# Optimization experiments

Measured on AMD Instinct MI355X. Metric: run time of the kernel, lower is better.

The kernel has to match this reference:

```python
import jax, jax.numpy as jnp
import numpy as np

B, H, W = 4, 512, 512
CIN, COUT = 3, 3
K = CIN + COUT  # 6x6 per-pixel Gaussian covariance factors


def setup_inputs() -> dict:
    key = jax.random.key(0)
    ks = jax.random.split(key, 6)
    x = jax.random.normal(ks[0], (B, CIN, H, W), jnp.float32)
    y = jax.random.normal(ks[1], (B, COUT, H, W), jnp.float32)
    m = jax.random.normal(ks[2], (B, K, H, W), jnp.float32)
    S = jax.random.normal(ks[3], (B, H, W, K, K), jnp.float32)
    I = jnp.eye(K, dtype=jnp.float32)
    # well-conditioned factors so linalg.inv is stable
    R = I + 0.1 * jax.random.normal(ks[4], (B, H, W, K, K), jnp.float32)
    D = 2.0 * I + 0.1 * jax.random.normal(ks[5], (B, H, W, K, K), jnp.float32)
    return {"x": x, "y": y, "m": m, "S": S, "R": R, "D": D}


def reference(x, y, m, S, R, D):
    C = CIN
    # get_my_by_x: S^{-1} = R D^{-1} R^T, per-pixel 6x6
    D_1 = jnp.linalg.inv(D)                      # [B,H,W,K,K]
    RT = jnp.swapaxes(R, -1, -2)
    S_1 = R @ D_1 @ RT                           # [B,H,W,K,K]
    Sxx = S_1[..., :C, :C]
    Syx = S_1[..., C:, :C]
    Q = Syx @ jnp.linalg.inv(Sxx)                # [B,H,W,COUT,CIN]
    mx = m[:, :C]
    my = m[:, C:]
    y_ = my + jnp.einsum('bijmn,bnij->bmij', Q, x - mx)  # [B,COUT,H,W]
    # reflect first 3 coords in the R-basis
    z = jnp.concatenate([x, y_], axis=1) - m     # [B,K,H,W]
    z = jnp.einsum('bmij,bijmn->bnij', z, RT)
    z = z.at[:, :3].multiply(-1.0)               # hardcoded :3 as in source
    z = jnp.einsum('bmij,bijmn->bnij', z, R) + m
    x_ = z[:, :3]
    y_out = z[:, 3:]
    S_out = jnp.transpose(S, (0, 3, 4, 1, 2))    # [B,K,K,H,W]
    return (x_, y_out, m, S_out)
```

## Files before the change

### kernel.cpp

```cpp
#include <hip/hip_runtime.h>

#define HWC (512 * 512)
#define BATCH 4
#define NPIX (BATCH * HWC)


typedef float f4 __attribute__((ext_vector_type(4)));

#define GLOAD(dst, addr, off) \
    asm volatile("global_load_dwordx4 %0, %1, off offset:" #off \
                 : "=v"(dst) : "v"(addr))

#define SOLVE6(w0,w1,w2,w3,w4,w5, o0,o1,o2,o3,o4,o5)                      \
  {                                                                       \
    float t0 = (w0);                                                      \
    float t1 = (w1) - l10*t0;                                             \
    float t2 = (w2) - l20*t0 - l21*t1;                                    \
    float t3 = (w3) - l30*t0 - l31*t1 - l32*t2;                           \
    float t4 = (w4) - l40*t0 - l41*t1 - l42*t2 - l43*t3;                  \
    float t5 = (w5) - l50*t0 - l51*t1 - l52*t2 - l53*t3 - l54*t4;         \
    o5 = t5*rd5;                                                          \
    o4 = (t4 - d45*o5)*rd4;                                               \
    o3 = (t3 - d34*o4 - d35*o5)*rd3;                                      \
    o2 = (t2 - d23*o3 - d24*o4 - d25*o5)*rd2;                             \
    o1 = (t1 - d12*o2 - d13*o3 - d14*o4 - d15*o5)*rd1;                    \
    o0 = (t0 - d01*o1 - d02*o2 - d03*o3 - d04*o4 - d05*o5)*rd0;           \
  }

#define S1(i,c) (r##i##0*X0_##c + r##i##1*X1_##c + r##i##2*X2_##c +       \
                 r##i##3*X3_##c + r##i##4*X4_##c + r##i##5*X5_##c)

__global__ __launch_bounds__(256, 2) void gpenc_fused(
    const float* __restrict__ x,
    const float* __restrict__ m,
    const float* __restrict__ S,
    const float* __restrict__ R,
    const float* __restrict__ Dm,
    float* __restrict__ xout,
    float* __restrict__ yout,
    float* __restrict__ mout,
    float* __restrict__ Sout)
{
    const int g = blockIdx.x * 256 + threadIdx.x;
    const int b = g >> 18;
    const int p = g & (HWC - 1);

    const size_t xb = (size_t)b * 3 * HWC + p;
    const size_t mb = (size_t)b * 6 * HWC + p;
    float xv0 = x[xb], xv1 = x[xb + (size_t)HWC], xv2 = x[xb + 2*(size_t)HWC];
    float mv0 = m[mb],                 mv1 = m[mb + (size_t)HWC],   mv2 = m[mb + 2*(size_t)HWC];
    float mv3 = m[mb + 3*(size_t)HWC], mv4 = m[mb + 4*(size_t)HWC], mv5 = m[mb + 5*(size_t)HWC];

    const float* sp = S  + (size_t)g * 36;
    const float* dp = Dm + (size_t)g * 36;
    const float* rp = R  + (size_t)g * 36;

    f4 s0,s1,s2,s3,s4,s5,s6,s7,s8;
    f4 q0,q1,q2,q3,q4,q5,q6,q7,q8;
    f4 p0,p1,p2,p3,p4,p5,p6,p7,p8;

    GLOAD(s0, sp, 0);   GLOAD(s1, sp, 16);  GLOAD(s2, sp, 32);
    GLOAD(s3, sp, 48);  GLOAD(s4, sp, 64);  GLOAD(s5, sp, 80);
    GLOAD(s6, sp, 96);  GLOAD(s7, sp, 112); GLOAD(s8, sp, 128);

    GLOAD(q0, dp, 0);   GLOAD(q1, dp, 16);  GLOAD(q2, dp, 32);
    GLOAD(q3, dp, 48);  GLOAD(q4, dp, 64);  GLOAD(q5, dp, 80);
    GLOAD(q6, dp, 96);  GLOAD(q7, dp, 112); GLOAD(q8, dp, 128);

    GLOAD(p0, rp, 0);   GLOAD(p1, rp, 16);  GLOAD(p2, rp, 32);
    GLOAD(p3, rp, 48);  GLOAD(p4, rp, 64);  GLOAD(p5, rp, 80);
    GLOAD(p6, rp, 96);  GLOAD(p7, rp, 112); GLOAD(p8, rp, 128);

    asm volatile("s_waitcnt vmcnt(0)" ::: "memory");
    __builtin_amdgcn_sched_barrier(0);

    float* so = Sout + (size_t)b * 36 * HWC + p;
    so[0*(size_t)HWC]  = s0.x; so[1*(size_t)HWC]  = s0.y; so[2*(size_t)HWC]  = s0.z; so[3*(size_t)HWC]  = s0.w;
    so[4*(size_t)HWC]  = s1.x; so[5*(size_t)HWC]  = s1.y; so[6*(size_t)HWC]  = s1.z; so[7*(size_t)HWC]  = s1.w;
    so[8*(size_t)HWC]  = s2.x; so[9*(size_t)HWC]  = s2.y; so[10*(size_t)HWC] = s2.z; so[11*(size_t)HWC] = s2.w;
    so[12*(size_t)HWC] = s3.x; so[13*(size_t)HWC] = s3.y; so[14*(size_t)HWC] = s3.z; so[15*(size_t)HWC] = s3.w;
    so[16*(size_t)HWC] = s4.x; so[17*(size_t)HWC] = s4.y; so[18*(size_t)HWC] = s4.z; so[19*(size_t)HWC] = s4.w;
    so[20*(size_t)HWC] = s5.x; so[21*(size_t)HWC] = s5.y; so[22*(size_t)HWC] = s5.z; so[23*(size_t)HWC] = s5.w;
    so[24*(size_t)HWC] = s6.x; so[25*(size_t)HWC] = s6.y; so[26*(size_t)HWC] = s6.z; so[27*(size_t)HWC] = s6.w;
    so[28*(size_t)HWC] = s7.x; so[29*(size_t)HWC] = s7.y; so[30*(size_t)HWC] = s7.z; so[31*(size_t)HWC] = s7.w;
    so[32*(size_t)HWC] = s8.x; so[33*(size_t)HWC] = s8.y; so[34*(size_t)HWC] = s8.z; so[35*(size_t)HWC] = s8.w;

    float d00=q0.x, d01=q0.y, d02=q0.z, d03=q0.w;
    float d04=q1.x, d05=q1.y, d10=q1.z, d11=q1.w;
    float d12=q2.x, d13=q2.y, d14=q2.z, d15=q2.w;
    float d20=q3.x, d21=q3.y, d22=q3.z, d23=q3.w;
    float d24=q4.x, d25=q4.y, d30=q4.z, d31=q4.w;
    float d32=q5.x, d33=q5.y, d34=q5.z, d35=q5.w;
    float d40=q6.x, d41=q6.y, d42=q6.z, d43=q6.w;
    float d44=q7.x, d45=q7.y, d50=q7.z, d51=q7.w;
    float d52=q8.x, d53=q8.y, d54=q8.z, d55=q8.w;

    float r00=p0.x, r01=p0.y, r02=p0.z, r03=p0.w;
    float r04=p1.x, r05=p1.y, r10=p1.z, r11=p1.w;
    float r12=p2.x, r13=p2.y, r14=p2.z, r15=p2.w;
    float r20=p3.x, r21=p3.y, r22=p3.z, r23=p3.w;
    float r24=p4.x, r25=p4.y, r30=p4.z, r31=p4.w;
    float r32=p5.x, r33=p5.y, r34=p5.z, r35=p5.w;
    float r40=p6.x, r41=p6.y, r42=p6.z, r43=p6.w;
    float r44=p7.x, r45=p7.y, r50=p7.z, r51=p7.w;
    float r52=p8.x, r53=p8.y, r54=p8.z, r55=p8.w;

    float rd0 = 1.0f/d00;
    float l10 = d10*rd0;
    d11 -= l10*d01; d12 -= l10*d02; d13 -= l10*d03; d14 -= l10*d04; d15 -= l10*d05;
    float l20 = d20*rd0;
    d21 -= l20*d01; d22 -= l20*d02; d23 -= l20*d03; d24 -= l20*d04; d25 -= l20*d05;
    float l30 = d30*rd0;
    d31 -= l30*d01; d32 -= l30*d02; d33 -= l30*d03; d34 -= l30*d04; d35 -= l30*d05;
    float l40 = d40*rd0;
    d41 -= l40*d01; d42 -= l40*d02; d43 -= l40*d03; d44 -= l40*d04; d45 -= l40*d05;
    float l50 = d50*rd0;
    d51 -= l50*d01; d52 -= l50*d02; d53 -= l50*d03; d54 -= l50*d04; d55 -= l50*d05;

    float rd1 = 1.0f/d11;
    float l21 = d21*rd1;
    d22 -= l21*d12; d23 -= l21*d13; d24 -= l21*d14; d25 -= l21*d15;
    float l31 = d31*rd1;
    d32 -= l31*d12; d33 -= l31*d13; d34 -= l31*d14; d35 -= l31*d15;
    float l41 = d41*rd1;
    d42 -= l41*d12; d43 -= l41*d13; d44 -= l41*d14; d45 -= l41*d15;
    float l51 = d51*rd1;
    d52 -= l51*d12; d53 -= l51*d13; d54 -= l51*d14; d55 -= l51*d15;

    float rd2 = 1.0f/d22;
    float l32 = d32*rd2;
    d33 -= l32*d23; d34 -= l32*d24; d35 -= l32*d25;
    float l42 = d42*rd2;
    d43 -= l42*d23; d44 -= l42*d24; d45 -= l42*d25;
    float l52 = d52*rd2;
    d53 -= l52*d23; d54 -= l52*d24; d55 -= l52*d25;

    float rd3 = 1.0f/d33;
    float l43 = d43*rd3;
    d44 -= l43*d34; d45 -= l43*d35;
    float l53 = d53*rd3;
    d54 -= l53*d34; d55 -= l53*d35;

    float rd4 = 1.0f/d44;
    float l54 = d54*rd4;
    d55 -= l54*d45;
    float rd5 = 1.0f/d55;

    float X0_0,X1_0,X2_0,X3_0,X4_0,X5_0;
    float X0_1,X1_1,X2_1,X3_1,X4_1,X5_1;
    float X0_2,X1_2,X2_2,X3_2,X4_2,X5_2;
    SOLVE6(r00,r01,r02,r03,r04,r05, X0_0,X1_0,X2_0,X3_0,X4_0,X5_0);
    SOLVE6(r10,r11,r12,r13,r14,r15, X0_1,X1_1,X2_1,X3_1,X4_1,X5_1);
    SOLVE6(r20,r21,r22,r23,r24,r25, X0_2,X1_2,X2_2,X3_2,X4_2,X5_2);

    float a00=S1(0,0), a01=S1(0,1), a02=S1(0,2);
    float a10=S1(1,0), a11=S1(1,1), a12=S1(1,2);
    float a20=S1(2,0), a21=S1(2,1), a22=S1(2,2);
    float b00=S1(3,0), b01=S1(3,1), b02=S1(3,2);
    float b10=S1(4,0), b11=S1(4,1), b12=S1(4,2);
    float b20=S1(5,0), b21=S1(5,1), b22=S1(5,2);

    float c00 =  (a11*a22 - a12*a21);
    float c01 = -(a10*a22 - a12*a20);
    float c02 =  (a10*a21 - a11*a20);
    float det = a00*c00 + a01*c01 + a02*c02;
    float rdet = 1.0f / det;
    float i00 = c00*rdet;
    float i01 = -(a01*a22 - a02*a21)*rdet;
    float i02 =  (a01*a12 - a02*a11)*rdet;
    float i10 = c01*rdet;
    float i11 =  (a00*a22 - a02*a20)*rdet;
    float i12 = -(a00*a12 - a02*a10)*rdet;
    float i20 = c02*rdet;
    float i21 = -(a00*a21 - a01*a20)*rdet;
    float i22 =  (a00*a11 - a01*a10)*rdet;

    float Q00 = b00*i00 + b01*i10 + b02*i20;
    float Q01 = b00*i01 + b01*i11 + b02*i21;
    float Q02 = b00*i02 + b01*i12 + b02*i22;
    float Q10 = b10*i00 + b11*i10 + b12*i20;
    float Q11 = b10*i01 + b11*i11 + b12*i21;
    float Q12 = b10*i02 + b11*i12 + b12*i22;
    float Q20 = b20*i00 + b21*i10 + b22*i20;
    float Q21 = b20*i01 + b21*i11 + b22*i21;
    float Q22 = b20*i02 + b21*i12 + b22*i22;

    float z0 = xv0 - mv0, z1v = xv1 - mv1, z2v = xv2 - mv2;
    float z3 = Q00*z0 + Q01*z1v + Q02*z2v;
    float z4 = Q10*z0 + Q11*z1v + Q12*z2v;
    float z5 = Q20*z0 + Q21*z1v + Q22*z2v;

    float w0 = -(r00*z0 + r01*z1v + r02*z2v + r03*z3 + r04*z4 + r05*z5);
    float w1 = -(r10*z0 + r11*z1v + r12*z2v + r13*z3 + r14*z4 + r15*z5);
    float w2 = -(r20*z0 + r21*z1v + r22*z2v + r23*z3 + r24*z4 + r25*z5);
    float w3 =  (r30*z0 + r31*z1v + r32*z2v + r33*z3 + r34*z4 + r35*z5);
    float w4 =  (r40*z0 + r41*z1v + r42*z2v + r43*z3 + r44*z4 + r45*z5);
    float w5 =  (r50*z0 + r51*z1v + r52*z2v + r53*z3 + r54*z4 + r55*z5);

    float o0 = w0*r00 + w1*r10 + w2*r20 + w3*r30 + w4*r40 + w5*r50 + mv0;
    float o1 = w0*r01 + w1*r11 + w2*r21 + w3*r31 + w4*r41 + w5*r51 + mv1;
    float o2 = w0*r02 + w1*r12 + w2*r22 + w3*r32 + w4*r42 + w5*r52 + mv2;
    float o3 = w0*r03 + w1*r13 + w2*r23 + w3*r33 + w4*r43 + w5*r53 + mv3;
    float o4 = w0*r04 + w1*r14 + w2*r24 + w3*r34 + w4*r44 + w5*r54 + mv4;
    float o5 = w0*r05 + w1*r15 + w2*r25 + w3*r35 + w4*r45 + w5*r55 + mv5;

    xout[xb] = o0; xout[xb + (size_t)HWC] = o1; xout[xb + 2*(size_t)HWC] = o2;
    yout[xb] = o3; yout[xb + (size_t)HWC] = o4; yout[xb + 2*(size_t)HWC] = o5;
    mout[mb]                    = mv0;
    mout[mb + (size_t)HWC]      = mv1;
    mout[mb + 2*(size_t)HWC]    = mv2;
    mout[mb + 3*(size_t)HWC]    = mv3;
    mout[mb + 4*(size_t)HWC]    = mv4;
    mout[mb + 5*(size_t)HWC]    = mv5;
}

extern "C" void kernel_launch(void* const* d_in, const int* in_sizes, int n_in,
                              void* d_out, int out_size, void* d_ws, size_t ws_size,
                              hipStream_t stream) {
    const float* x  = (const float*)d_in[0];
    const float* m  = (const float*)d_in[2];
    const float* S  = (const float*)d_in[3];
    const float* R  = (const float*)d_in[4];
    const float* D  = (const float*)d_in[5];

    float* out = (float*)d_out;
    const size_t N3 = (size_t)BATCH * 3 * HWC;
    const size_t N6 = (size_t)BATCH * 6 * HWC;
    float* xout = out;
    float* yout = out + N3;
    float* mout = out + 2 * N3;
    float* Sout = out + 2 * N3 + N6;

    gpenc_fused<<<NPIX / 256, 256, 0, stream>>>(x, m, S, R, D,
                                                xout, yout, mout, Sout);
}
```

Before: 138.2 us.

## Transpose S through LDS for vectorized coalesced Sout stores

Each thread's 36 S values are staged into a padded shared-memory tile. After a block barrier, each wave writes contiguous float4 segments of the transposed Sout layout, replacing 36 scalar strided stores per thread. The kernel now waits only for the D loads before compute and raises the occupancy hint from 2 to 3 blocks per CU. The cost is about 37 KB of LDS per block and a __syncthreads, which may limit occupancy and add register pressure.

```diff
diff --git a/kernel.cpp b/kernel.cpp
--- a/kernel.cpp
+++ b/kernel.cpp
@@ -30,7 +30,9 @@
 #define S1(i,c) (r##i##0*X0_##c + r##i##1*X1_##c + r##i##2*X2_##c +       \
                  r##i##3*X3_##c + r##i##4*X4_##c + r##i##5*X5_##c)
 
-__global__ __launch_bounds__(256, 2) void gpenc_fused(
+#define LROW 260
+
+__global__ __launch_bounds__(256, 3) void gpenc_fused(
     const float* __restrict__ x,
     const float* __restrict__ m,
     const float* __restrict__ S,
@@ -41,9 +43,17 @@
     float* __restrict__ mout,
     float* __restrict__ Sout)
 {
-    const int g = blockIdx.x * 256 + threadIdx.x;
+    __shared__ float lds[36 * LROW];
+
+    const int t = threadIdx.x;
+    const int g = blockIdx.x * 256 + t;
     const int b = g >> 18;
     const int p = g & (HWC - 1);
+    const int pixbase = (blockIdx.x & 1023) * 256;
+
+    const f4* S4 = reinterpret_cast<const f4*>(S + (size_t)g * 36);
+    f4 s0 = S4[0], s1 = S4[1], s2 = S4[2], s3 = S4[3], s4 = S4[4],
+       s5 = S4[5], s6 = S4[6], s7 = S4[7], s8 = S4[8];
 
     const size_t xb = (size_t)b * 3 * HWC + p;
     const size_t mb = (size_t)b * 6 * HWC + p;
@@ -51,39 +61,42 @@
     float mv0 = m[mb],                 mv1 = m[mb + (size_t)HWC],   mv2 = m[mb + 2*(size_t)HWC];
     float mv3 = m[mb + 3*(size_t)HWC], mv4 = m[mb + 4*(size_t)HWC], mv5 = m[mb + 5*(size_t)HWC];
 
-    const float* sp = S  + (size_t)g * 36;
+    lds[ 0*LROW + t] = s0.x; lds[ 1*LROW + t] = s0.y; lds[ 2*LROW + t] = s0.z; lds[ 3*LROW + t] = s0.w;
+    lds[ 4*LROW + t] = s1.x; lds[ 5*LROW + t] = s1.y; lds[ 6*LROW + t] = s1.z; lds[ 7*LROW + t] = s1.w;
+    lds[ 8*LROW + t] = s2.x; lds[ 9*LROW + t] = s2.y; lds[10*LROW + t] = s2.z; lds[11*LROW + t] = s2.w;
+    lds[12*LROW + t] = s3.x; lds[13*LROW + t] = s3.y; lds[14*LROW + t] = s3.z; lds[15*LROW + t] = s3.w;
+    lds[16*LROW + t] = s4.x; lds[17*LROW + t] = s4.y; lds[18*LROW + t] = s4.z; lds[19*LROW + t] = s4.w;
+    lds[20*LROW + t] = s5.x; lds[21*LROW + t] = s5.y; lds[22*LROW + t] = s5.z; lds[23*LROW + t] = s5.w;
+    lds[24*LROW + t] = s6.x; lds[25*LROW + t] = s6.y; lds[26*LROW + t] = s6.z; lds[27*LROW + t] = s6.w;
+    lds[28*LROW + t] = s7.x; lds[29*LROW + t] = s7.y; lds[30*LROW + t] = s7.z; lds[31*LROW + t] = s7.w;
+    lds[32*LROW + t] = s8.x; lds[33*LROW + t] = s8.y; lds[34*LROW + t] = s8.z; lds[35*LROW + t] = s8.w;
+
     const float* dp = Dm + (size_t)g * 36;
     const float* rp = R  + (size_t)g * 36;
-
-    f4 s0,s1,s2,s3,s4,s5,s6,s7,s8;
     f4 q0,q1,q2,q3,q4,q5,q6,q7,q8;
     f4 p0,p1,p2,p3,p4,p5,p6,p7,p8;
-
-    GLOAD(s0, sp, 0);   GLOAD(s1, sp, 16);  GLOAD(s2, sp, 32);
-    GLOAD(s3, sp, 48);  GLOAD(s4, sp, 64);  GLOAD(s5, sp, 80);
-    GLOAD(s6, sp, 96);  GLOAD(s7, sp, 112); GLOAD(s8, sp, 128);
-
     GLOAD(q0, dp, 0);   GLOAD(q1, dp, 16);  GLOAD(q2, dp, 32);
     GLOAD(q3, dp, 48);  GLOAD(q4, dp, 64);  GLOAD(q5, dp, 80);
     GLOAD(q6, dp, 96);  GLOAD(q7, dp, 112); GLOAD(q8, dp, 128);
-
     GLOAD(p0, rp, 0);   GLOAD(p1, rp, 16);  GLOAD(p2, rp, 32);
     GLOAD(p3, rp, 48);  GLOAD(p4, rp, 64);  GLOAD(p5, rp, 80);
     GLOAD(p6, rp, 96);  GLOAD(p7, rp, 112); GLOAD(p8, rp, 128);
 
-    asm volatile("s_waitcnt vmcnt(0)" ::: "memory");
+    __syncthreads();
+    {
+        const int w = t >> 6, l = t & 63;
+        const f4* lds4 = reinterpret_cast<const f4*>(lds);
+        float* so = Sout + (size_t)b * 36 * HWC + pixbase + 4 * l;
+#pragma unroll
+        for (int s = 0; s < 9; ++s) {
+            const int j = s * 4 + w;
+            f4 v = lds4[j * (LROW / 4) + l];
+            *reinterpret_cast<f4*>(so + (size_t)j * HWC) = v;
+        }
+    }
+
+    asm volatile("s_waitcnt vmcnt(9)" ::: "memory");
     __builtin_amdgcn_sched_barrier(0);
-
-    float* so = Sout + (size_t)b * 36 * HWC + p;
-    so[0*(size_t)HWC]  = s0.x; so[1*(size_t)HWC]  = s0.y; so[2*(size_t)HWC]  = s0.z; so[3*(size_t)HWC]  = s0.w;
-    so[4*(size_t)HWC]  = s1.x; so[5*(size_t)HWC]  = s1.y; so[6*(size_t)HWC]  = s1.z; so[7*(size_t)HWC]  = s1.w;
-    so[8*(size_t)HWC]  = s2.x; so[9*(size_t)HWC]  = s2.y; so[10*(size_t)HWC] = s2.z; so[11*(size_t)HWC] = s2.w;
-    so[12*(size_t)HWC] = s3.x; so[13*(size_t)HWC] = s3.y; so[14*(size_t)HWC] = s3.z; so[15*(size_t)HWC] = s3.w;
-    so[16*(size_t)HWC] = s4.x; so[17*(size_t)HWC] = s4.y; so[18*(size_t)HWC] = s4.z; so[19*(size_t)HWC] = s4.w;
-    so[20*(size_t)HWC] = s5.x; so[21*(size_t)HWC] = s5.y; so[22*(size_t)HWC] = s5.z; so[23*(size_t)HWC] = s5.w;
-    so[24*(size_t)HWC] = s6.x; so[25*(size_t)HWC] = s6.y; so[26*(size_t)HWC] = s6.z; so[27*(size_t)HWC] = s6.w;
-    so[28*(size_t)HWC] = s7.x; so[29*(size_t)HWC] = s7.y; so[30*(size_t)HWC] = s7.z; so[31*(size_t)HWC] = s7.w;
-    so[32*(size_t)HWC] = s8.x; so[33*(size_t)HWC] = s8.y; so[34*(size_t)HWC] = s8.z; so[35*(size_t)HWC] = s8.w;
 
     float d00=q0.x, d01=q0.y, d02=q0.z, d03=q0.w;
     float d04=q1.x, d05=q1.y, d10=q1.z, d11=q1.w;
```

New measurement: 136.2 us. About the same (-1.4%).
